# Performance work log

Measured on AMD Instinct MI355X. Metric: run time of the kernel, lower is better.

Reference implementation:

```python
import jax, jax.numpy as jnp
import numpy as np

N = 100000
E = 3200000
D = 512

def setup_inputs() -> dict:
    key = jax.random.key(0)
    ks = jax.random.split(key, 6)
    X = jax.random.normal(ks[0], (N, D), dtype=jnp.float32)
    edge_row = jax.random.randint(ks[1], (E,), 0, N, dtype=jnp.int32)
    edge_col = jax.random.randint(ks[2], (E,), 0, N, dtype=jnp.int32)
    edge_val = jax.random.uniform(ks[3], (E,), dtype=jnp.float32)
    # glorot-uniform-ish init for weights
    lim = (6.0 / (D + D)) ** 0.5
    W1 = jax.random.uniform(ks[4], (D, D), dtype=jnp.float32, minval=-lim, maxval=lim)
    W2 = jax.random.uniform(ks[5], (D, D), dtype=jnp.float32, minval=-lim, maxval=lim)
    return {"X": X, "edge_row": edge_row, "edge_col": edge_col,
            "edge_val": edge_val, "W1": W1, "W2": W2}

def _spmm(edge_row, edge_col, edge_val, H):
    # out[r] = sum_{e: row[e]==r} val[e] * H[col[e]]
    msgs = edge_val[:, None] * H[edge_col]          # [E, D]
    return jax.ops.segment_sum(msgs, edge_row, num_segments=N)

def reference(X, edge_row, edge_col, edge_val, W1, W2):
    # layer 1: An @ (X @ W1), tanh activation, no bias
    h = jnp.tanh(_spmm(edge_row, edge_col, edge_val, X @ W1))
    # layer 2
    h = jnp.tanh(_spmm(edge_row, edge_col, edge_val, h @ W2))
    # tf.nn.l2_normalize(curr, axis=1)
    norm = jnp.sqrt(jnp.maximum(jnp.sum(h * h, axis=1, keepdims=True), 1e-12))
    return h / norm
```

## Files before the change

kernel.cpp:

```cpp
#include <hip/hip_runtime.h>
#include <hip/hip_fp16.h>

#define D_DIM 512

typedef __attribute__((ext_vector_type(8))) _Float16 half8;
typedef __attribute__((ext_vector_type(4))) float f32x4;
typedef __attribute__((ext_vector_type(2))) float float2v;

__device__ inline unsigned short f16b(float f) {
  return __half_as_ushort(__float2half(f));
}



__global__ __launch_bounds__(256) void k_hist(const int* __restrict__ row, int* __restrict__ cnt, int E) {
  int i = blockIdx.x * blockDim.x + threadIdx.x;
  if (i < E) atomicAdd(&cnt[row[i]], 1);
}

__global__ __launch_bounds__(1024) void k_scanA(const int* __restrict__ cnt, int* __restrict__ rp,
                                                int* __restrict__ bsum, int n) {
  __shared__ int s[1024];
  int i = blockIdx.x * 1024 + threadIdx.x;
  int v = (i < n) ? cnt[i] : 0;
  s[threadIdx.x] = v;
  __syncthreads();
  for (int off = 1; off < 1024; off <<= 1) {
    int t = (threadIdx.x >= off) ? s[threadIdx.x - off] : 0;
    __syncthreads();
    s[threadIdx.x] += t;
    __syncthreads();
  }
  if (i < n) rp[i] = s[threadIdx.x] - v;
  if (threadIdx.x == 1023) bsum[blockIdx.x] = s[1023];
}

__global__ __launch_bounds__(1024) void k_scanB(int* __restrict__ bsum, int nb) {
  __shared__ int s[1024];
  int v = (threadIdx.x < nb) ? bsum[threadIdx.x] : 0;
  s[threadIdx.x] = v;
  __syncthreads();
  for (int off = 1; off < 1024; off <<= 1) {
    int t = (threadIdx.x >= off) ? s[threadIdx.x - off] : 0;
    __syncthreads();
    s[threadIdx.x] += t;
    __syncthreads();
  }
  if (threadIdx.x < nb) bsum[threadIdx.x] = s[threadIdx.x] - v;
}

__global__ __launch_bounds__(256) void k_scanC(int* __restrict__ rp, const int* __restrict__ bsum, int n, int E) {
  int i = blockIdx.x * 256 + threadIdx.x;
  if (i < n) rp[i] += bsum[i >> 10];
  if (i == 0) rp[n] = E;
}

__global__ __launch_bounds__(256) void k_scatter(const int* __restrict__ row, const int* __restrict__ col,
                                                 const float* __restrict__ val, int* __restrict__ cur,
                                                 int2* __restrict__ edat, int E) {
  int i = blockIdx.x * blockDim.x + threadIdx.x;
  if (i < E) {
    int r = row[i];
    int p = atomicAdd(&cur[r], 1);
    edat[p] = make_int2(col[i], __float_as_int(val[i]));
  }
}


__global__ __launch_bounds__(256) void k_convA(const float* __restrict__ X, unsigned* __restrict__ Xf,
                                               long nValid4, long nTot4) {
  long i = (long)blockIdx.x * 256 + threadIdx.x;
  long stride = (long)gridDim.x * 256;
  for (; i < nTot4; i += stride) {
    float4 x = make_float4(0.f, 0.f, 0.f, 0.f);
    if (i < nValid4) x = ((const float4*)X)[i];
    uint2 v;
    v.x = (unsigned)f16b(x.x) | ((unsigned)f16b(x.y) << 16);
    v.y = (unsigned)f16b(x.z) | ((unsigned)f16b(x.w) << 16);
    const long r = i >> 7;
    const int c0 = (int)(i & 127) * 4;
    const long halfidx = ((r >> 4) * 16 + (c0 >> 5)) * 512 + ((c0 >> 3) & 3) * 128 + (r & 15) * 8 + (c0 & 7);
    ((uint2*)Xf)[halfidx >> 2] = v;
  }
}


__global__ __launch_bounds__(256) void k_repackW(const float* __restrict__ W, _Float16* __restrict__ Wf) {
  int n = blockIdx.x * 256 + threadIdx.x;
  int kg = blockIdx.y;
  half8 v;
#pragma unroll
  for (int j = 0; j < 8; ++j) v[j] = (_Float16)W[(kg * 8 + j) * D_DIM + n];
  const long halfidx = ((long)(kg >> 2) * 32 + (n >> 4)) * 512 + (kg & 3) * 128 + (n & 15) * 8;
  *(half8*)(Wf + halfidx) = v;
}


__global__ __launch_bounds__(256) void k_gemm(const _Float16* __restrict__ A,
                                              const _Float16* __restrict__ B,
                                              _Float16* __restrict__ Cout, int MB) {
  const int id = blockIdx.x;
  const int xcd = id & 7;
  const int s = id >> 3;
  const int panel = (s >> 2) * 8 + xcd;
  if (panel >= MB) return;
  const int nb = s & 3;

  const int tid = threadIdx.x;
  const int lane = tid & 63;
  const int w = tid >> 6;
  const int wr = w >> 1, wc = w & 1;
  const int c = lane & 15, g = lane >> 4;
  const long r0 = (long)panel * 128 + wr * 64;
  const int n0 = nb * 128 + wc * 64;

  f32x4 acc[4][4] = {};

  const long aBase = ((r0 >> 4) * 16) * 512 + lane * 8;
  const long bBase = ((long)(n0 >> 4)) * 512 + lane * 8;

#pragma unroll 4
  for (int k0 = 0; k0 < D_DIM; k0 += 32) {
    const int k5 = k0 >> 5;
    half8 a[4], b[4];
#pragma unroll
    for (int m = 0; m < 4; ++m) a[m] = *(const half8*)(A + aBase + (long)(m * 16 + k5) * 512);
#pragma unroll
    for (int nf = 0; nf < 4; ++nf)
      b[nf] = *(const half8*)(B + bBase + (long)(k5 * 32 + nf) * 512);
#pragma unroll
    for (int m = 0; m < 4; ++m)
#pragma unroll
      for (int nf = 0; nf < 4; ++nf)
        acc[m][nf] = __builtin_amdgcn_mfma_f32_16x16x32_f16(a[m], b[nf], acc[m][nf], 0, 0, 0);
  }

  __shared__ float ep[4][16][68];
#pragma unroll
  for (int m = 0; m < 4; ++m) {
#pragma unroll
    for (int nf = 0; nf < 4; ++nf)
#pragma unroll
      for (int j = 0; j < 4; ++j)
        ep[w][g * 4 + j][nf * 16 + c] = acc[m][nf][j];
    __syncthreads();
    {
      const int row = lane >> 2;
      const int ch = lane & 3;
      float v[16];
#pragma unroll
      for (int q = 0; q < 16; ++q) v[q] = ep[w][row][ch * 16 + q];
      half8 h0, h1;
#pragma unroll
      for (int q = 0; q < 8; ++q) {
        h0[q] = (_Float16)v[q];
        h1[q] = (_Float16)v[8 + q];
      }
      _Float16* dst = Cout + (r0 + m * 16 + row) * D_DIM + n0 + ch * 16;
      *(half8*)dst = h0;
      *(half8*)(dst + 8) = h1;
    }
    __syncthreads();
  }
}


template <int MODE>
__global__ __launch_bounds__(256) void k_spmm(const unsigned short* __restrict__ T, const int* __restrict__ rp,
                                              const int2* __restrict__ edat,
                                              unsigned* __restrict__ Hf, float* __restrict__ out) {
  __shared__ float p[4][D_DIM];
  __shared__ float wss[4];
  const int r = blockIdx.x;
  const int tid = threadIdx.x;
  const int w = tid >> 6, lane = tid & 63;
  const int beg = rp[r], end = rp[r + 1];
  const int cnt = end - beg;
  const int eb = beg + ((cnt * w) >> 2);
  const int ee = beg + ((cnt * (w + 1)) >> 2);

  float acc[8] = {};
  const uint4* Tv = (const uint4*)T;
  for (int e = eb; e < ee; ++e) {
    const int2 ed = edat[e];
    const int ccol = ed.x;
    const float v = __int_as_float(ed.y);
    uint4 x = Tv[(long)ccol * 64 + lane];
    unsigned xs[4] = {x.x, x.y, x.z, x.w};
#pragma unroll
    for (int q = 0; q < 4; ++q) {
      float2 f = __half22float2(__builtin_bit_cast(__half2, xs[q]));
      acc[2 * q] = fmaf(v, f.x, acc[2 * q]);
      acc[2 * q + 1] = fmaf(v, f.y, acc[2 * q + 1]);
    }
  }
  *(float4*)&p[w][lane * 8] = make_float4(acc[0], acc[1], acc[2], acc[3]);
  *(float4*)&p[w][lane * 8 + 4] = make_float4(acc[4], acc[5], acc[6], acc[7]);
  __syncthreads();

  const int c = tid * 2;
  float s0 = p[0][c] + p[1][c] + p[2][c] + p[3][c];
  float s1 = p[0][c + 1] + p[1][c + 1] + p[2][c + 1] + p[3][c + 1];
  s0 = tanhf(s0);
  s1 = tanhf(s1);

  if (MODE == 0) {
    unsigned hv = (unsigned)f16b(s0) | ((unsigned)f16b(s1) << 16);
    const long halfidx = ((long)(r >> 4) * 16 + (c >> 5)) * 512 + ((c >> 3) & 3) * 128 + (r & 15) * 8 + (c & 7);
    __builtin_nontemporal_store(hv, Hf + (halfidx >> 1));
  } else {
    float ss = fmaf(s0, s0, s1 * s1);
#pragma unroll
    for (int off = 1; off < 64; off <<= 1) ss += __shfl_xor(ss, off);
    if (lane == 0) wss[w] = ss;
    __syncthreads();
    const float tot = wss[0] + wss[1] + wss[2] + wss[3];
    const float sc = rsqrtf(fmaxf(tot, 1e-12f));
    float2v o;
    o.x = s0 * sc;
    o.y = s1 * sc;
    __builtin_nontemporal_store(o, (float2v*)out + (long)r * 256 + tid);
  }
}


extern "C" void kernel_launch(void* const* d_in, const int* in_sizes, int n_in,
                              void* d_out, int out_size, void* d_ws, size_t ws_size,
                              hipStream_t stream) {
  const float* X = (const float*)d_in[0];
  const int* erow = (const int*)d_in[1];
  const int* ecol = (const int*)d_in[2];
  const float* evalv = (const float*)d_in[3];
  const float* W1 = (const float*)d_in[4];
  const float* W2 = (const float*)d_in[5];
  const int N = in_sizes[0] / D_DIM;
  const int E = in_sizes[1];
  (void)n_in; (void)out_size; (void)ws_size;

  const int MB = (N + 127) / 128;
  const long Mp = (long)MB * 128;

  char* wsp = (char*)d_ws;
  size_t off = 0;
  auto alloc = [&](size_t bytes) {
    void* p = wsp + off;
    off = (off + bytes + 255) & ~(size_t)255;
    return p;
  };
  unsigned short* T  = (unsigned short*)alloc(Mp * D_DIM * 2);
  unsigned* Af = (unsigned*)alloc(Mp * D_DIM * 2);
  int2* edat  = (int2*)alloc((size_t)E * 8);
  int* rowptr = (int*)alloc((size_t)(N + 1) * 4);
  int* cursor = (int*)alloc((size_t)N * 4);
  int* bsum   = (int*)alloc(1024 * 4);
  _Float16* W1f = (_Float16*)alloc((size_t)D_DIM * D_DIM * 2);
  _Float16* W2f = (_Float16*)alloc((size_t)D_DIM * D_DIM * 2);

  const int nScanBlk = (N + 1023) / 1024;
  const int gemmGrid = 32 * ((MB + 7) / 8);

  hipMemsetAsync(cursor, 0, (size_t)N * 4, stream);
  k_hist<<<dim3((E + 255) / 256), dim3(256), 0, stream>>>(erow, cursor, E);
  k_scanA<<<dim3(nScanBlk), dim3(1024), 0, stream>>>(cursor, rowptr, bsum, N);
  k_scanB<<<dim3(1), dim3(1024), 0, stream>>>(bsum, nScanBlk);
  k_scanC<<<dim3((N + 255) / 256), dim3(256), 0, stream>>>(rowptr, bsum, N, E);
  hipMemcpyAsync(cursor, rowptr, (size_t)N * 4, hipMemcpyDeviceToDevice, stream);
  k_scatter<<<dim3((E + 255) / 256), dim3(256), 0, stream>>>(erow, ecol, evalv, cursor, edat, E);

  k_convA<<<dim3(4096), dim3(256), 0, stream>>>(X, Af, (long)N * D_DIM / 4, Mp * D_DIM / 4);
  k_repackW<<<dim3(2, 64), dim3(256), 0, stream>>>(W1, W1f);
  k_repackW<<<dim3(2, 64), dim3(256), 0, stream>>>(W2, W2f);

  k_gemm<<<dim3(gemmGrid), dim3(256), 0, stream>>>((const _Float16*)Af, W1f, (_Float16*)T, MB);
  k_spmm<0><<<dim3(N), dim3(256), 0, stream>>>(T, rowptr, edat, Af, nullptr);
  k_gemm<<<dim3(gemmGrid), dim3(256), 0, stream>>>((const _Float16*)Af, W2f, (_Float16*)T, MB);
  k_spmm<1><<<dim3(N), dim3(256), 0, stream>>>(T, rowptr, edat, nullptr, (float*)d_out);
}
```

Measured before the change: 1.563 ms.

## Stage GEMM tiles through LDS with async loads and split layer-1 SpMM by column halves

The GEMM now stages A and B tiles into shared memory with global_load_lds in a double buffer. This lets the four waves share loaded fragments instead of each wave reading its own from global memory, and lets the next k-step load overlap the MFMAs. The layer-1 SpMM is split into two launches, each covering 256 columns. The goal is to shrink the gathered working set of T per pass so it fits better in cache. The split costs an extra pass over the edge list and row pointers, plus narrower 8-byte gathers and 2-byte scattered stores.

```diff
diff --git a/kernel.cpp b/kernel.cpp
--- a/kernel.cpp
+++ b/kernel.cpp
@@ -11,6 +11,12 @@
   return __half_as_ushort(__float2half(f));
 }
 
+
+__device__ inline void glds16(const _Float16* g, _Float16* l) {
+  __builtin_amdgcn_global_load_lds(
+      (const __attribute__((address_space(1))) void*)g,
+      (__attribute__((address_space(3))) void*)l, 16, 0, 0);
+}
 
 
 __global__ __launch_bounds__(256) void k_hist(const int* __restrict__ row, int* __restrict__ cnt, int E) {
@@ -101,10 +107,10 @@
                                               _Float16* __restrict__ Cout, int MB) {
   const int id = blockIdx.x;
   const int xcd = id & 7;
-  const int s = id >> 3;
-  const int panel = (s >> 2) * 8 + xcd;
+  const int sgrid = id >> 3;
+  const int panel = (sgrid >> 2) * 8 + xcd;
   if (panel >= MB) return;
-  const int nb = s & 3;
+  const int nb = sgrid & 3;
 
   const int tid = threadIdx.x;
   const int lane = tid & 63;
@@ -114,28 +120,53 @@
   const long r0 = (long)panel * 128 + wr * 64;
   const int n0 = nb * 128 + wc * 64;
 
+  __shared__ __align__(16) char smem[32768];
+
   f32x4 acc[4][4] = {};
 
-  const long aBase = ((r0 >> 4) * 16) * 512 + lane * 8;
-  const long bBase = ((long)(n0 >> 4)) * 512 + lane * 8;
-
-#pragma unroll 4
-  for (int k0 = 0; k0 < D_DIM; k0 += 32) {
-    const int k5 = k0 >> 5;
+  const int f0 = w, f1 = w + 4;
+  const long aSrc0 = ((long)(panel * 8 + f0) * 16) * 512 + lane * 8;
+  const long aSrc1 = ((long)(panel * 8 + f1) * 16) * 512 + lane * 8;
+  const long bSrcBase = ((long)nb * 8) * 512 + lane * 8;
+
+  {
+    _Float16* Ad = (_Float16*)smem;
+    _Float16* Bd = (_Float16*)(smem + 8192);
+    glds16(A + aSrc0, Ad + f0 * 512);
+    glds16(A + aSrc1, Ad + f1 * 512);
+    glds16(B + bSrcBase + (long)f0 * 512, Bd + f0 * 512);
+    glds16(B + bSrcBase + (long)f1 * 512, Bd + f1 * 512);
+  }
+  __syncthreads();
+
+  int cur = 0;
+  for (int s = 0; s < 16; ++s) {
+    if (s < 15) {
+      const int k5 = s + 1;
+      _Float16* Ad = (_Float16*)(smem + (cur ^ 1) * 16384);
+      _Float16* Bd = (_Float16*)(smem + (cur ^ 1) * 16384 + 8192);
+      glds16(A + aSrc0 + (long)k5 * 512, Ad + f0 * 512);
+      glds16(A + aSrc1 + (long)k5 * 512, Ad + f1 * 512);
+      glds16(B + bSrcBase + ((long)k5 * 32 + f0) * 512, Bd + f0 * 512);
+      glds16(B + bSrcBase + ((long)k5 * 32 + f1) * 512, Bd + f1 * 512);
+    }
+    const _Float16* As = (const _Float16*)(smem + cur * 16384);
+    const _Float16* Bs = (const _Float16*)(smem + cur * 16384 + 8192);
     half8 a[4], b[4];
 #pragma unroll
-    for (int m = 0; m < 4; ++m) a[m] = *(const half8*)(A + aBase + (long)(m * 16 + k5) * 512);
-#pragma unroll
-    for (int nf = 0; nf < 4; ++nf)
-      b[nf] = *(const half8*)(B + bBase + (long)(k5 * 32 + nf) * 512);
-#pragma unroll
-    for (int m = 0; m < 4; ++m)
-#pragma unroll
-      for (int nf = 0; nf < 4; ++nf)
-        acc[m][nf] = __builtin_amdgcn_mfma_f32_16x16x32_f16(a[m], b[nf], acc[m][nf], 0, 0, 0);
-  }
-
-  __shared__ float ep[4][16][68];
+    for (int mi = 0; mi < 4; ++mi) a[mi] = *(const half8*)(As + (wr * 4 + mi) * 512 + lane * 8);
+#pragma unroll
+    for (int ni = 0; ni < 4; ++ni) b[ni] = *(const half8*)(Bs + (wc * 4 + ni) * 512 + lane * 8);
+#pragma unroll
+    for (int mi = 0; mi < 4; ++mi)
+#pragma unroll
+      for (int ni = 0; ni < 4; ++ni)
+        acc[mi][ni] = __builtin_amdgcn_mfma_f32_16x16x32_f16(a[mi], b[ni], acc[mi][ni], 0, 0, 0);
+    __syncthreads();
+    cur ^= 1;
+  }
+
+  float (*ep)[16][68] = (float (*)[16][68])smem;
 #pragma unroll
   for (int m = 0; m < 4; ++m) {
 #pragma unroll
@@ -165,10 +196,43 @@
 }
 
 
-template <int MODE>
-__global__ __launch_bounds__(256) void k_spmm(const unsigned short* __restrict__ T, const int* __restrict__ rp,
-                                              const int2* __restrict__ edat,
-                                              unsigned* __restrict__ Hf, float* __restrict__ out) {
+__global__ __launch_bounds__(256) void k_spmmH(const unsigned short* __restrict__ T, const int* __restrict__ rp,
+                                               const int2* __restrict__ edat,
+                                               unsigned short* __restrict__ Hf, int d0) {
+  __shared__ float p[4][256];
+  const int r = blockIdx.x;
+  const int tid = threadIdx.x;
+  const int w = tid >> 6, lane = tid & 63;
+  const int beg = rp[r], end = rp[r + 1];
+  const int cnt = end - beg;
+  const int eb = beg + ((cnt * w) >> 2);
+  const int ee = beg + ((cnt * (w + 1)) >> 2);
+
+  float acc[4] = {};
+  for (int e = eb; e < ee; ++e) {
+    const int2 ed = edat[e];
+    const float v = __int_as_float(ed.y);
+    uint2 x = *(const uint2*)(T + (long)ed.x * D_DIM + d0 + lane * 4);
+    float2 f0 = __half22float2(__builtin_bit_cast(__half2, x.x));
+    float2 f1 = __half22float2(__builtin_bit_cast(__half2, x.y));
+    acc[0] = fmaf(v, f0.x, acc[0]);
+    acc[1] = fmaf(v, f0.y, acc[1]);
+    acc[2] = fmaf(v, f1.x, acc[2]);
+    acc[3] = fmaf(v, f1.y, acc[3]);
+  }
+  *(float4*)&p[w][lane * 4] = make_float4(acc[0], acc[1], acc[2], acc[3]);
+  __syncthreads();
+
+  const int cg = d0 + tid;
+  float s = p[0][tid] + p[1][tid] + p[2][tid] + p[3][tid];
+  s = tanhf(s);
+  const long halfidx = ((long)(r >> 4) * 16 + (cg >> 5)) * 512 + ((cg >> 3) & 3) * 128 + (r & 15) * 8 + (cg & 7);
+  __builtin_nontemporal_store(f16b(s), Hf + halfidx);
+}
+
+
+__global__ __launch_bounds__(256) void k_spmm1(const unsigned short* __restrict__ T, const int* __restrict__ rp,
+                                               const int2* __restrict__ edat, float* __restrict__ out) {
   __shared__ float p[4][D_DIM];
   __shared__ float wss[4];
   const int r = blockIdx.x;
@@ -183,9 +247,8 @@
   const uint4* Tv = (const uint4*)T;
   for (int e = eb; e < ee; ++e) {
     const int2 ed = edat[e];
-    const int ccol = ed.x;
     const float v = __int_as_float(ed.y);
-    uint4 x = Tv[(long)ccol * 64 + lane];
+    uint4 x = Tv[(long)ed.x * 64 + lane];
     unsigned xs[4] = {x.x, x.y, x.z, x.w};
 #pragma unroll
     for (int q = 0; q < 4; ++q) {
@@ -204,23 +267,17 @@
   s0 = tanhf(s0);
   s1 = tanhf(s1);
 
-  if (MODE == 0) {
-    unsigned hv = (unsigned)f16b(s0) | ((unsigned)f16b(s1) << 16);
-    const long halfidx = ((long)(r >> 4) * 16 + (c >> 5)) * 512 + ((c >> 3) & 3) * 128 + (r & 15) * 8 + (c & 7);
-    __builtin_nontemporal_store(hv, Hf + (halfidx >> 1));
-  } else {
-    float ss = fmaf(s0, s0, s1 * s1);
-#pragma unroll
-    for (int off = 1; off < 64; off <<= 1) ss += __shfl_xor(ss, off);
-    if (lane == 0) wss[w] = ss;
-    __syncthreads();
-    const float tot = wss[0] + wss[1] + wss[2] + wss[3];
-    const float sc = rsqrtf(fmaxf(tot, 1e-12f));
-    float2v o;
-    o.x = s0 * sc;
-    o.y = s1 * sc;
-    __builtin_nontemporal_store(o, (float2v*)out + (long)r * 256 + tid);
-  }
+  float ss = fmaf(s0, s0, s1 * s1);
+#pragma unroll
+  for (int off = 1; off < 64; off <<= 1) ss += __shfl_xor(ss, off);
+  if (lane == 0) wss[w] = ss;
+  __syncthreads();
+  const float tot = wss[0] + wss[1] + wss[2] + wss[3];
+  const float sc = rsqrtf(fmaxf(tot, 1e-12f));
+  float2v o;
+  o.x = s0 * sc;
+  o.y = s1 * sc;
+  __builtin_nontemporal_store(o, (float2v*)out + (long)r * 256 + tid);
 }
 
 
@@ -272,7 +329,8 @@
   k_repackW<<<dim3(2, 64), dim3(256), 0, stream>>>(W2, W2f);
 
   k_gemm<<<dim3(gemmGrid), dim3(256), 0, stream>>>((const _Float16*)Af, W1f, (_Float16*)T, MB);
-  k_spmm<0><<<dim3(N), dim3(256), 0, stream>>>(T, rowptr, edat, Af, nullptr);
+  k_spmmH<<<dim3(N), dim3(256), 0, stream>>>(T, rowptr, edat, (unsigned short*)Af, 0);
+  k_spmmH<<<dim3(N), dim3(256), 0, stream>>>(T, rowptr, edat, (unsigned short*)Af, 256);
   k_gemm<<<dim3(gemmGrid), dim3(256), 0, stream>>>((const _Float16*)Af, W2f, (_Float16*)T, MB);
-  k_spmm<1><<<dim3(N), dim3(256), 0, stream>>>(T, rowptr, edat, nullptr, (float*)d_out);
-}
+  k_spmm1<<<dim3(N), dim3(256), 0, stream>>>(T, rowptr, edat, (float*)d_out);
+}
```

New measurement: 1.700 ms. 1.09x slower.

## Stage GEMM tiles in LDS via direct global-to-LDS loads

Applied to the files above, without the earlier changes.

The GEMM kernel now stages A and B fragments into shared memory with global_load_lds (16-byte direct loads), and each wave then reads its MFMA operands from LDS. Previously every wave loaded its operands straight from global memory, so fragments shared between waves were fetched twice. The epilogue scratch buffer reuses the same shared allocation. The loop is single-buffered with two barriers per step, so load latency is not overlapped with compute, and occupancy may drop due to 32KB of LDS per block.

```diff
diff --git a/kernel.cpp b/kernel.cpp
--- a/kernel.cpp
+++ b/kernel.cpp
@@ -11,6 +11,12 @@
   return __half_as_ushort(__float2half(f));
 }
 
+
+__device__ inline void glds16(const _Float16* g, _Float16* l) {
+  __builtin_amdgcn_global_load_lds(
+      (const __attribute__((address_space(1))) void*)g,
+      (__attribute__((address_space(3))) void*)l, 16, 0, 0);
+}
 
 
 __global__ __launch_bounds__(256) void k_hist(const int* __restrict__ row, int* __restrict__ cnt, int E) {
@@ -101,10 +107,10 @@
                                               _Float16* __restrict__ Cout, int MB) {
   const int id = blockIdx.x;
   const int xcd = id & 7;
-  const int s = id >> 3;
-  const int panel = (s >> 2) * 8 + xcd;
+  const int sgrid = id >> 3;
+  const int panel = (sgrid >> 2) * 8 + xcd;
   if (panel >= MB) return;
-  const int nb = s & 3;
+  const int nb = sgrid & 3;
 
   const int tid = threadIdx.x;
   const int lane = tid & 63;
@@ -114,28 +120,47 @@
   const long r0 = (long)panel * 128 + wr * 64;
   const int n0 = nb * 128 + wc * 64;
 
+  __shared__ __align__(16) char smem[32768];
+  _Float16* Asl = (_Float16*)smem;
+  _Float16* Bsl = (_Float16*)(smem + 16384);
+
   f32x4 acc[4][4] = {};
 
-  const long aBase = ((r0 >> 4) * 16) * 512 + lane * 8;
-  const long bBase = ((long)(n0 >> 4)) * 512 + lane * 8;
-
-#pragma unroll 4
-  for (int k0 = 0; k0 < D_DIM; k0 += 32) {
-    const int k5 = k0 >> 5;
-    half8 a[4], b[4];
-#pragma unroll
-    for (int m = 0; m < 4; ++m) a[m] = *(const half8*)(A + aBase + (long)(m * 16 + k5) * 512);
-#pragma unroll
-    for (int nf = 0; nf < 4; ++nf)
-      b[nf] = *(const half8*)(B + bBase + (long)(k5 * 32 + nf) * 512);
-#pragma unroll
-    for (int m = 0; m < 4; ++m)
-#pragma unroll
-      for (int nf = 0; nf < 4; ++nf)
-        acc[m][nf] = __builtin_amdgcn_mfma_f32_16x16x32_f16(a[m], b[nf], acc[m][nf], 0, 0, 0);
-  }
-
-  __shared__ float ep[4][16][68];
+  const int f0 = w, f1 = w + 4;
+  const long aF0 = ((long)(panel * 8 + f0) * 16) * 512 + lane * 8;
+  const long aF1 = ((long)(panel * 8 + f1) * 16) * 512 + lane * 8;
+  const long bBase = ((long)nb * 8) * 512 + lane * 8;
+
+  for (int s = 0; s < 8; ++s) {
+    const int k5a = 2 * s, k5b = 2 * s + 1;
+    glds16(A + aF0 + (long)k5a * 512, Asl + (0 * 8 + f0) * 512);
+    glds16(A + aF0 + (long)k5b * 512, Asl + (1 * 8 + f0) * 512);
+    glds16(A + aF1 + (long)k5a * 512, Asl + (0 * 8 + f1) * 512);
+    glds16(A + aF1 + (long)k5b * 512, Asl + (1 * 8 + f1) * 512);
+    glds16(B + bBase + ((long)k5a * 32 + f0) * 512, Bsl + (0 * 8 + f0) * 512);
+    glds16(B + bBase + ((long)k5b * 32 + f0) * 512, Bsl + (1 * 8 + f0) * 512);
+    glds16(B + bBase + ((long)k5a * 32 + f1) * 512, Bsl + (0 * 8 + f1) * 512);
+    glds16(B + bBase + ((long)k5b * 32 + f1) * 512, Bsl + (1 * 8 + f1) * 512);
+    __syncthreads();
+#pragma unroll
+    for (int k5loc = 0; k5loc < 2; ++k5loc) {
+      half8 a[4], b[4];
+#pragma unroll
+      for (int mi = 0; mi < 4; ++mi)
+        a[mi] = *(const half8*)(Asl + (k5loc * 8 + wr * 4 + mi) * 512 + lane * 8);
+#pragma unroll
+      for (int ni = 0; ni < 4; ++ni)
+        b[ni] = *(const half8*)(Bsl + (k5loc * 8 + wc * 4 + ni) * 512 + lane * 8);
+#pragma unroll
+      for (int mi = 0; mi < 4; ++mi)
+#pragma unroll
+        for (int ni = 0; ni < 4; ++ni)
+          acc[mi][ni] = __builtin_amdgcn_mfma_f32_16x16x32_f16(a[mi], b[ni], acc[mi][ni], 0, 0, 0);
+    }
+    __syncthreads();
+  }
+
+  float (*ep)[16][68] = (float (*)[16][68])smem;
 #pragma unroll
   for (int m = 0; m < 4; ++m) {
 #pragma unroll
@@ -183,9 +208,8 @@
   const uint4* Tv = (const uint4*)T;
   for (int e = eb; e < ee; ++e) {
     const int2 ed = edat[e];
-    const int ccol = ed.x;
     const float v = __int_as_float(ed.y);
-    uint4 x = Tv[(long)ccol * 64 + lane];
+    uint4 x = Tv[(long)ed.x * 64 + lane];
     unsigned xs[4] = {x.x, x.y, x.z, x.w};
 #pragma unroll
     for (int q = 0; q < 4; ++q) {
```

New measurement: 1.504 ms. 3.8% less time.
